# Performance work log

Hardware: AMD Instinct MI355X
Metric: run time of the kernel (lower is better)

## Reference

```python
import jax, jax.numpy as jnp
import numpy as np

D_MODEL = 1024
NUM_HEADS = 16
HEAD_DIM = D_MODEL // NUM_HEADS


def setup_inputs() -> dict:
    key0 = jax.random.key(0)
    ks = jax.random.split(key0, 11)
    B, S = 8, 4096
    s = 0.02
    return {
        "query": jax.random.normal(ks[0], (B, S, D_MODEL), dtype=jnp.float32),
        "key": jax.random.normal(ks[1], (B, D_MODEL), dtype=jnp.float32),
        "value": jax.random.normal(ks[2], (B, D_MODEL), dtype=jnp.float32),
        "Wq": jax.random.normal(ks[3], (D_MODEL, D_MODEL), dtype=jnp.float32) * s,
        "bq": jnp.zeros((D_MODEL,), dtype=jnp.float32),
        "Wk": jax.random.normal(ks[4], (D_MODEL, HEAD_DIM), dtype=jnp.float32) * s,
        "bk": jnp.zeros((HEAD_DIM,), dtype=jnp.float32),
        "Wv": jax.random.normal(ks[5], (D_MODEL, HEAD_DIM), dtype=jnp.float32) * s,
        "bv": jnp.zeros((HEAD_DIM,), dtype=jnp.float32),
        "Wo": jax.random.normal(ks[6], (D_MODEL, D_MODEL), dtype=jnp.float32) * s,
        "bo": jnp.zeros((D_MODEL,), dtype=jnp.float32),
    }


def reference(query, key, value, Wq, bq, Wk, bk, Wv, bv, Wo, bo):
    B, S, _ = query.shape
    # Q: [B, H, S, hd]
    Q = (query @ Wq + bq).reshape(B, S, NUM_HEADS, HEAD_DIM).transpose(0, 2, 1, 3)
    # shared single K/V vector per batch: [B, hd]
    K = key @ Wk + bk
    V = value @ Wv + bv
    scale = 1.0 / np.sqrt(HEAD_DIM).astype(np.float32)
    # scores: [B, H, S, 1] (kv_len == 1)
    scores = jnp.einsum("bhsd,bd->bhs", Q, K)[..., None] * scale
    attn = jax.nn.softmax(scores, axis=-1)  # softmax over size-1 axis -> ones
    # attended: [B, H, S, hd] = attn * broadcast V
    attended = attn * V[:, None, None, :]
    attended = attended.transpose(0, 2, 1, 3).reshape(B, S, D_MODEL)
    return attended @ Wo + bo
```

## Files before the change

### kernel.cpp

```cpp
#include <hip/hip_runtime.h>


#define D_MODEL 1024
#define HEAD_DIM 64
#define B_SIZE 8
#define S_LEN 4096

typedef float vfloat4 __attribute__((ext_vector_type(4)));

__global__ __launch_bounds__(256) void k_outvec(
    const float* __restrict__ value, const float4* __restrict__ Wv4,
    const float4* __restrict__ bv4, const float* __restrict__ Wo,
    const float* __restrict__ bo, float* __restrict__ outv) {
  int b = blockIdx.x >> 4;
  int jc = blockIdx.x & 15;
  int jbase = jc * 64;
  int t = threadIdx.x;

  __shared__ __align__(16) float Vsh[64];
  {
    int d4 = t & 15;
    int kp = t >> 4;
    const float* vrow = value + b * D_MODEL;
    float4 acc = make_float4(0.f, 0.f, 0.f, 0.f);
    int k0 = kp * 64;
#pragma unroll 8
    for (int i = 0; i < 64; ++i) {
      int k = k0 + i;
      float v = vrow[k];
      float4 w = Wv4[k * 16 + d4];
      acc.x += v * w.x;
      acc.y += v * w.y;
      acc.z += v * w.z;
      acc.w += v * w.w;
    }
    __shared__ float4 red[16][16];
    red[kp][d4] = acc;
    __syncthreads();
    if (t < 16) {
      float4 s = bv4[t];
#pragma unroll
      for (int p = 0; p < 16; ++p) {
        float4 r = red[p][t];
        s.x += r.x;
        s.y += r.y;
        s.z += r.z;
        s.w += r.w;
      }
      ((float4*)Vsh)[t] = s;
    }
    __syncthreads();
  }

  int j = t & 63;
  int part = t >> 6;
  float acc = 0.f;
  int c0 = part * 256;
#pragma unroll 8
  for (int i = 0; i < 256; ++i) {
    int c = c0 + i;
    acc += Vsh[c & 63] * Wo[c * D_MODEL + jbase + j];
  }
  __shared__ float red2[4][64];
  red2[part][j] = acc;
  __syncthreads();
  if (t < 64) {
    outv[b * D_MODEL + jbase + t] =
        red2[0][t] + red2[1][t] + red2[2][t] + red2[3][t] + bo[jbase + t];
  }
}

__global__ __launch_bounds__(256) void k_broadcast(
    const vfloat4* __restrict__ vec4, vfloat4* __restrict__ out4) {
  int b = blockIdx.x >> 7;
  int g = blockIdx.x & 127;
  int t = threadIdx.x;
  vfloat4 v = vec4[b * 256 + t];
  vfloat4* p = out4 + (size_t)b * S_LEN * 256 + (size_t)g * 256 + t;
#pragma unroll 8
  for (int i = 0; i < 32; ++i) {
    __builtin_nontemporal_store(v, p);
    p += 128 * 256;
  }
}

extern "C" void kernel_launch(void* const* d_in, const int* in_sizes, int n_in,
                              void* d_out, int out_size, void* d_ws,
                              size_t ws_size, hipStream_t stream) {
  const float* value = (const float*)d_in[2];
  const float* Wv = (const float*)d_in[7];
  const float* bv = (const float*)d_in[8];
  const float* Wo = (const float*)d_in[9];
  const float* bo = (const float*)d_in[10];

  float* outv = (float*)d_ws;

  k_outvec<<<B_SIZE * 16, 256, 0, stream>>>(value, (const float4*)Wv,
                                            (const float4*)bv, Wo, bo, outv);
  k_broadcast<<<B_SIZE * 128, 256, 0, stream>>>((const vfloat4*)outv,
                                                (vfloat4*)d_out);
}
```

Baseline: 243.6 us.

## Fuse output-vector computation and broadcast store into a single kernel

Merges the per-batch output vector computation and the broadcast write into one kernel. Each block computes a 64-column slice of the output vector and writes it across half of the sequence rows, which removes one launch and the workspace round trip. In exchange the V and output-vector math is done twice per slice, only 256 blocks issue the 128 MB of stores, and each wavefront's store row covers just 256 bytes instead of full 4 KB rows, which may hurt write bandwidth.

```diff
diff --git a/kernel.cpp b/kernel.cpp
--- a/kernel.cpp
+++ b/kernel.cpp
@@ -8,16 +8,22 @@
 
 typedef float vfloat4 __attribute__((ext_vector_type(4)));
 
-__global__ __launch_bounds__(256) void k_outvec(
+__global__ __launch_bounds__(256) void k_fused(
     const float* __restrict__ value, const float4* __restrict__ Wv4,
     const float4* __restrict__ bv4, const float* __restrict__ Wo,
-    const float* __restrict__ bo, float* __restrict__ outv) {
-  int b = blockIdx.x >> 4;
-  int jc = blockIdx.x & 15;
+    const float* __restrict__ bo, vfloat4* __restrict__ out4) {
+  int bx = blockIdx.x;
+  int b = bx >> 5;
+  int jc = (bx >> 1) & 15;
+  int sh = bx & 1;
   int jbase = jc * 64;
   int t = threadIdx.x;
 
   __shared__ __align__(16) float Vsh[64];
+  __shared__ float4 red[16][16];
+  __shared__ float red2[4][64];
+  __shared__ __align__(16) float outSh[64];
+
   {
     int d4 = t & 15;
     int kp = t >> 4;
@@ -34,7 +40,6 @@
       acc.z += v * w.z;
       acc.w += v * w.w;
     }
-    __shared__ float4 red[16][16];
     red[kp][d4] = acc;
     __syncthreads();
     if (t < 16) {
@@ -52,35 +57,36 @@
     __syncthreads();
   }
 
-  int j = t & 63;
-  int part = t >> 6;
-  float acc = 0.f;
-  int c0 = part * 256;
+  {
+    int j = t & 63;
+    int part = t >> 6;
+    float acc = 0.f;
+    int c0 = part * 256;
 #pragma unroll 8
-  for (int i = 0; i < 256; ++i) {
-    int c = c0 + i;
-    acc += Vsh[c & 63] * Wo[c * D_MODEL + jbase + j];
+    for (int i = 0; i < 256; ++i) {
+      int c = c0 + i;
+      acc += Vsh[c & 63] * Wo[c * D_MODEL + jbase + j];
+    }
+    red2[part][j] = acc;
+    __syncthreads();
+    if (t < 64) {
+      outSh[t] =
+          red2[0][t] + red2[1][t] + red2[2][t] + red2[3][t] + bo[jbase + t];
+    }
+    __syncthreads();
   }
-  __shared__ float red2[4][64];
-  red2[part][j] = acc;
-  __syncthreads();
-  if (t < 64) {
-    outv[b * D_MODEL + jbase + t] =
-        red2[0][t] + red2[1][t] + red2[2][t] + red2[3][t] + bo[jbase + t];
-  }
-}
 
-__global__ __launch_bounds__(256) void k_broadcast(
-    const vfloat4* __restrict__ vec4, vfloat4* __restrict__ out4) {
-  int b = blockIdx.x >> 7;
-  int g = blockIdx.x & 127;
-  int t = threadIdx.x;
-  vfloat4 v = vec4[b * 256 + t];
-  vfloat4* p = out4 + (size_t)b * S_LEN * 256 + (size_t)g * 256 + t;
+  {
+    int lane4 = t & 15;
+    int r = t >> 4;
+    vfloat4 v = ((const vfloat4*)outSh)[lane4];
+    size_t s0 = (size_t)sh * 2048 + r;
+    vfloat4* p = out4 + ((size_t)b * S_LEN + s0) * 256 + jc * 16 + lane4;
 #pragma unroll 8
-  for (int i = 0; i < 32; ++i) {
-    __builtin_nontemporal_store(v, p);
-    p += 128 * 256;
+    for (int i = 0; i < 128; ++i) {
+      __builtin_nontemporal_store(v, p);
+      p += 16 * 256;
+    }
   }
 }
 
@@ -93,10 +99,7 @@
   const float* Wo = (const float*)d_in[9];
   const float* bo = (const float*)d_in[10];
 
-  float* outv = (float*)d_ws;
-
-  k_outvec<<<B_SIZE * 16, 256, 0, stream>>>(value, (const float4*)Wv,
-                                            (const float4*)bv, Wo, bo, outv);
-  k_broadcast<<<B_SIZE * 128, 256, 0, stream>>>((const vfloat4*)outv,
-                                                (vfloat4*)d_out);
+  k_fused<<<B_SIZE * 16 * 2, 256, 0, stream>>>(value, (const float4*)Wv,
+                                               (const float4*)bv, Wo, bo,
+                                               (vfloat4*)d_out);
 }
```

Result: no change. 247.8 us (+1.7%).
